# Kernel tuning notes

Hardware: AMD Instinct MI355X
Metric: run time of the kernel (lower is better)

Reference implementation:

```python
import jax, jax.numpy as jnp
import numpy as np

B, S, H, I, E = 2, 1024, 1024, 4096, 8

def setup_inputs() -> dict:
    key = jax.random.key(0)
    ks = jax.random.split(key, 8)
    s_h = 1.0 / np.sqrt(H)
    s_i = 1.0 / np.sqrt(I)
    return {
        "x": jax.random.normal(ks[0], (B, S, H), dtype=jnp.float32),
        "router_w": jax.random.uniform(ks[1], (H, E), jnp.float32, -s_h, s_h),
        "router_b": jax.random.uniform(ks[2], (E,), jnp.float32, -s_h, s_h),
        "w1": jax.random.uniform(ks[3], (E, H, I), jnp.float32, -s_h, s_h),
        "b1": jax.random.uniform(ks[4], (E, I), jnp.float32, -s_h, s_h),
        "w2": jax.random.uniform(ks[5], (E, I, H), jnp.float32, -s_i, s_i),
        "b2": jax.random.uniform(ks[6], (E, H), jnp.float32, -s_i, s_i),
        "game_emb": jax.random.normal(ks[7], (E, H), dtype=jnp.float32) * 0.02,
    }

def reference(x, router_w, router_b, w1, b1, w2, b2, game_emb):
    # Router: top-1 expert per token (softmax is monotone, argmax of logits)
    logits = jnp.einsum('bsh,he->bse', x, router_w) + router_b  # [B,S,E]
    expert_idx = jnp.argmax(logits, axis=-1)                    # [B,S] int
    out = jnp.zeros_like(x)
    n_experts = w1.shape[0]
    for e in range(n_experts):  # fixed small expert loop
        mask = (expert_idx == e)[..., None]                     # [B,S,1]
        sel = x + 0.1 * game_emb[e]                             # embedding add
        h = jax.nn.gelu(jnp.einsum('bsh,hi->bsi', sel, w1[e]) + b1[e], approximate=False)
        y = jnp.einsum('bsi,ih->bsh', h, w2[e]) + b2[e]
        out = jnp.where(mask, y, out)                           # scatter combine
    return out
```

## Files before the change

kernel.cpp:

```cpp
#include <hip/hip_runtime.h>
#include <hip/hip_bf16.h>
#include <math.h>

#define HDIM 1024
#define IDIM 4096
#define NE 8
#define NTOK 2048
#define PADROWS 256

typedef __attribute__((ext_vector_type(8))) short bf16x8;
typedef __attribute__((ext_vector_type(4))) float f32x4;

__device__ __forceinline__ unsigned int f2bf(float f) {
    unsigned int u = __float_as_uint(f);
    u = (u + 0x7FFFu + ((u >> 16) & 1u)) >> 16;
    return u;
}

__device__ __forceinline__ unsigned int pkbf2(float lo, float hi) {
    union { __hip_bfloat162 h; unsigned int u; } cv;
    cv.h = __float22bfloat162_rn(make_float2(lo, hi));
    return cv.u;
}

__device__ __forceinline__ float comp4(const float4& v, int c) {
    return c == 0 ? v.x : c == 1 ? v.y : c == 2 ? v.z : v.w;
}

__device__ __forceinline__ int swz8(int i) { return (i ^ (i >> 3)) & 7; }

__device__ __forceinline__ float gelu_erf(float v) {
    float x = v * 0.70710678118654752f;
    float ax = fabsf(x);
    float t = 1.0f / (1.0f + 0.3275911f * ax);
    float p = t * (0.254829592f + t * (-0.284496736f + t * (1.421413741f +
              t * (-1.453152027f + t * 1.061405429f))));
    float er = 1.0f - p * __expf(-x * x);
    er = copysignf(er, v);
    return 0.5f * v * (1.0f + er);
}

template<typename T, typename U>
__device__ __forceinline__ void gld16(const T* g, U* l) {
    __builtin_amdgcn_global_load_lds((const __attribute__((address_space(1))) void*)g,
                                     (__attribute__((address_space(3))) void*)l, 16, 0, 0);
}

__global__ __launch_bounds__(256) void router_k(const float* __restrict__ x,
                                                const float* __restrict__ rw,
                                                const float* __restrict__ rb,
                                                int* __restrict__ eidx,
                                                int* __restrict__ counts) {
    const int wave = threadIdx.x >> 6, lane = threadIdx.x & 63;
    const int t = blockIdx.x * 4 + wave;
    if (t >= NTOK) return;
    double acc[NE];
#pragma unroll
    for (int e = 0; e < NE; e++) acc[e] = 0.0;
    for (int h = lane; h < HDIM; h += 64) {
        double xv = (double)x[(size_t)t * HDIM + h];
        const float4* rwp = (const float4*)&rw[h * NE];
        float4 r0 = rwp[0], r1 = rwp[1];
        acc[0] += xv * (double)r0.x;  acc[1] += xv * (double)r0.y;
        acc[2] += xv * (double)r0.z;  acc[3] += xv * (double)r0.w;
        acc[4] += xv * (double)r1.x;  acc[5] += xv * (double)r1.y;
        acc[6] += xv * (double)r1.z;  acc[7] += xv * (double)r1.w;
    }
#pragma unroll
    for (int m = 32; m >= 1; m >>= 1) {
#pragma unroll
        for (int e = 0; e < NE; e++) acc[e] += __shfl_xor(acc[e], m);
    }
    if (lane == 0) {
        double best = acc[0] + (double)rb[0];
        int be = 0;
#pragma unroll
        for (int e = 1; e < NE; e++) {
            double v = acc[e] + (double)rb[e];
            if (v > best) { best = v; be = e; }
        }
        eidx[t] = be;
        atomicAdd(&counts[be], 1);
    }
}

__global__ void scan_k(const int* __restrict__ counts, int* __restrict__ offsets) {
    if (threadIdx.x == 0 && blockIdx.x == 0) {
        int s = 0;
        for (int e = 0; e < NE; e++) { offsets[e] = s; s += counts[e]; }
        offsets[NE] = s;
    }
}

__global__ __launch_bounds__(256) void gather_k(const float* __restrict__ x,
                                                const float* __restrict__ gemb,
                                                const int* __restrict__ eidx,
                                                const int* __restrict__ offsets,
                                                int* __restrict__ cursors,
                                                int* __restrict__ rowmap,
                                                unsigned short* __restrict__ Xg) {
    __shared__ int srow, se;
    const int t = blockIdx.x;
    if (threadIdx.x == 0) {
        int e = eidx[t];
        int pos = atomicAdd(&cursors[e], 1);
        int row = offsets[e] + pos;
        rowmap[row] = t;
        srow = row; se = e;
    }
    __syncthreads();
    const int row = srow, e = se;
    const int c = threadIdx.x * 4;
    float4 xv = *(const float4*)&x[(size_t)t * HDIM + c];
    float4 gv = *(const float4*)&gemb[(size_t)e * HDIM + c];
    ushort4 o;
    o.x = (unsigned short)f2bf(xv.x + 0.1f * gv.x);
    o.y = (unsigned short)f2bf(xv.y + 0.1f * gv.y);
    o.z = (unsigned short)f2bf(xv.z + 0.1f * gv.z);
    o.w = (unsigned short)f2bf(xv.w + 0.1f * gv.w);
    *(ushort4*)&Xg[(size_t)row * HDIM + c] = o;
}

template<int EPI>
__global__ __launch_bounds__(256, 3) void moe_gemm_k(
        const unsigned short* __restrict__ A, int lda, int Kfull, int ksplit,
        const float* __restrict__ Bw, int ldbN,
        const float* __restrict__ bias,
        const int* __restrict__ offsets, const int* __restrict__ rowmap,
        unsigned short* __restrict__ Hout, float* __restrict__ Yout,
        float* __restrict__ P, size_t pstride) {
    __shared__ __align__(16) unsigned short At[2][128 * 64];
    __shared__ __align__(16) unsigned short Bt[128 * 64];

    const int e = blockIdx.z & 7;
    const int split = blockIdx.z >> 3;
    const int rend = offsets[e + 1];
    const int r0 = offsets[e] + blockIdx.y * 128;
    if (r0 >= rend) return;
    const int c0 = blockIdx.x * 128;
    const int kbeg = split * ksplit;
    const int nt = ksplit / 64;
    const float* Be = Bw + (size_t)e * Kfull * ldbN;

    const int tid = threadIdx.x;
    const int wave = tid >> 6, lane = tid & 63;
    const int wr = (wave >> 1) * 64, wc = (wave & 1) * 64;
    const int l15 = lane & 15, l4 = lane >> 4;

    const int bcol = (tid & 31) * 4;
    const int boct = tid >> 5;
    const float* bsrc = Be + (size_t)boct * 8 * ldbN + c0 + bcol;
    int bwo[4];
#pragma unroll
    for (int i = 0; i < 4; ++i) {
        int col = bcol + i;
        bwo[i] = col * 64 + (boct ^ swz8(col)) * 8;
    }

    const unsigned short* adsrc[4];
    int adoff[4];
#pragma unroll
    for (int p = 0; p < 4; ++p) {
        int gidx = p * 256 + tid;
        int row = gidx >> 3, ps = gidx & 7;
        adsrc[p] = A + (size_t)(r0 + row) * lda + (ps ^ swz8(row)) * 8;
        adoff[p] = gidx * 8;
    }

    float4 fv[8];
    auto loadB = [&](int kabs) {
#pragma unroll
        for (int j = 0; j < 8; ++j)
            fv[j] = *(const float4*)&bsrc[(size_t)(kabs + j) * ldbN];
    };
    auto dmaA = [&](int kabs, int buf) {
#pragma unroll
        for (int p = 0; p < 4; ++p)
            gld16(adsrc[p] + kabs, &At[buf][adoff[p]]);
    };

    f32x4 acc[4][4];
#pragma unroll
    for (int m = 0; m < 4; ++m)
#pragma unroll
        for (int n = 0; n < 4; ++n) acc[m][n] = (f32x4){0.f, 0.f, 0.f, 0.f};

    loadB(kbeg);
    dmaA(kbeg, 0);
    for (int t = 0; t < nt; ++t) {
        const int cur = t & 1;
#pragma unroll
        for (int i = 0; i < 4; ++i) {
            uint4 w;
            w.x = pkbf2(comp4(fv[0], i), comp4(fv[1], i));
            w.y = pkbf2(comp4(fv[2], i), comp4(fv[3], i));
            w.z = pkbf2(comp4(fv[4], i), comp4(fv[5], i));
            w.w = pkbf2(comp4(fv[6], i), comp4(fv[7], i));
            *(uint4*)&Bt[bwo[i]] = w;
        }
        if (t + 1 < nt) {
            loadB(kbeg + (t + 1) * 64);
            dmaA(kbeg + (t + 1) * 64, cur ^ 1);
            asm volatile("s_waitcnt vmcnt(12) lgkmcnt(0)" ::: "memory");
        } else {
            asm volatile("s_waitcnt vmcnt(0) lgkmcnt(0)" ::: "memory");
        }
        __builtin_amdgcn_s_barrier();
        __builtin_amdgcn_sched_barrier(0);
#pragma unroll
        for (int kh = 0; kh < 2; ++kh) {
            const int kb = kh * 4 + l4;
            bf16x8 af[4], bfr[4];
#pragma unroll
            for (int m = 0; m < 4; ++m) {
                int row = wr + m * 16 + l15;
                af[m] = *(const bf16x8*)&At[cur][row * 64 + (kb ^ swz8(row)) * 8];
            }
#pragma unroll
            for (int n = 0; n < 4; ++n) {
                int col = wc + n * 16 + l15;
                bfr[n] = *(const bf16x8*)&Bt[col * 64 + (kb ^ swz8(col)) * 8];
            }
#pragma unroll
            for (int m = 0; m < 4; ++m)
#pragma unroll
                for (int n = 0; n < 4; ++n)
                    acc[m][n] = __builtin_amdgcn_mfma_f32_16x16x32_bf16(af[m], bfr[n], acc[m][n], 0, 0, 0);
        }
        __builtin_amdgcn_sched_barrier(0);
        __builtin_amdgcn_s_barrier();
        __builtin_amdgcn_sched_barrier(0);
    }

#pragma unroll
    for (int m = 0; m < 4; ++m) {
#pragma unroll
        for (int r = 0; r < 4; ++r) {
            const int row = r0 + wr + m * 16 + l4 * 4 + r;
            if (row < rend) {
                if constexpr (EPI == 0) {
#pragma unroll
                    for (int n = 0; n < 4; ++n) {
                        int col = c0 + wc + n * 16 + l15;
                        float v = acc[m][n][r] + bias[(size_t)e * ldbN + col];
                        Hout[(size_t)row * IDIM + col] = (unsigned short)f2bf(gelu_erf(v));
                    }
                } else if (split == 0) {
                    const int tt = rowmap[row];
#pragma unroll
                    for (int n = 0; n < 4; ++n) {
                        int col = c0 + wc + n * 16 + l15;
                        Yout[(size_t)tt * HDIM + col] = acc[m][n][r] + bias[(size_t)e * ldbN + col];
                    }
                } else {
                    float* Ps = P + (size_t)(split - 1) * pstride;
#pragma unroll
                    for (int n = 0; n < 4; ++n) {
                        int col = c0 + wc + n * 16 + l15;
                        Ps[(size_t)row * HDIM + col] = acc[m][n][r];
                    }
                }
            }
        }
    }
}

__global__ __launch_bounds__(256) void reduce_k(const float* __restrict__ P,
                                                size_t pstride, int nparts,
                                                const int* __restrict__ rowmap,
                                                float* __restrict__ out) {
    const int row = blockIdx.x;
    const int t = rowmap[row];
    const int c = threadIdx.x * 4;
    f32x4 s = *(const f32x4*)&out[(size_t)t * HDIM + c];
    for (int p = 0; p < nparts; ++p)
        s += *(const f32x4*)&P[(size_t)p * pstride + (size_t)row * HDIM + c];
    *(f32x4*)&out[(size_t)t * HDIM + c] = s;
}

extern "C" void kernel_launch(void* const* d_in, const int* in_sizes, int n_in,
                              void* d_out, int out_size, void* d_ws, size_t ws_size,
                              hipStream_t stream) {
    const float* x    = (const float*)d_in[0];
    const float* rw   = (const float*)d_in[1];
    const float* rb   = (const float*)d_in[2];
    const float* w1   = (const float*)d_in[3];
    const float* b1   = (const float*)d_in[4];
    const float* w2   = (const float*)d_in[5];
    const float* b2   = (const float*)d_in[6];
    const float* gemb = (const float*)d_in[7];
    float* out = (float*)d_out;

    char* ws = (char*)d_ws;
    int* meta    = (int*)ws;
    int* counts  = meta;
    int* cursors = meta + 8;
    int* offsets = meta + 16;
    int* eidx    = meta + 32;
    int* rowmap  = meta + 32 + NTOK;
    size_t off = 32768;
    unsigned short* Xg = (unsigned short*)(ws + off);
    off += (size_t)(NTOK + PADROWS) * HDIM * 2;
    unsigned short* Hbuf = (unsigned short*)(ws + off);
    off += (size_t)(NTOK + PADROWS) * IDIM * 2;
    float* P = (float*)(ws + off);
    const size_t pstride = (size_t)NTOK * HDIM;
    int nsplit = 1;
    if (ws_size >= off + 3 * pstride * 4) nsplit = 4;
    else if (ws_size >= off + 1 * pstride * 4) nsplit = 2;

    hipMemsetAsync(counts, 0, 16 * sizeof(int), stream);
    router_k<<<NTOK / 4, 256, 0, stream>>>(x, rw, rb, eidx, counts);
    scan_k<<<1, 64, 0, stream>>>(counts, offsets);
    gather_k<<<NTOK, 256, 0, stream>>>(x, gemb, eidx, offsets, cursors, rowmap, Xg);
    moe_gemm_k<0><<<dim3(IDIM / 128, 3, NE), 256, 0, stream>>>(
        Xg, HDIM, HDIM, HDIM, w1, IDIM, b1, offsets, rowmap, Hbuf, nullptr, nullptr, 0);
    moe_gemm_k<1><<<dim3(HDIM / 128, 3, NE * nsplit), 256, 0, stream>>>(
        Hbuf, IDIM, IDIM, IDIM / nsplit, w2, HDIM, b2, offsets, rowmap, nullptr, out, P, pstride);
    if (nsplit > 1)
        reduce_k<<<NTOK, 256, 0, stream>>>(P, pstride, nsplit - 1, rowmap, out);
}
```

Before: 193.6 us.

## Prefetch second-layer expert weights into cache during first GEMM

The first expert GEMM now issues extra global-to-LDS loads that sweep the whole w2 weight tensor into a dummy shared buffer. The aim is to warm the large last-level cache so the second GEMM reads w2 from cache instead of HBM. This adds memory traffic and in-flight loads to the first GEMM, which may already be bandwidth-bound. Blocks that exit early skip their share of the prefetch.

```diff
diff --git a/kernel.cpp b/kernel.cpp
--- a/kernel.cpp
+++ b/kernel.cpp
@@ -121,16 +121,18 @@
     *(ushort4*)&Xg[(size_t)row * HDIM + c] = o;
 }
 
-template<int EPI>
+template<int EPI, int TOUCH>
 __global__ __launch_bounds__(256, 3) void moe_gemm_k(
         const unsigned short* __restrict__ A, int lda, int Kfull, int ksplit,
         const float* __restrict__ Bw, int ldbN,
         const float* __restrict__ bias,
         const int* __restrict__ offsets, const int* __restrict__ rowmap,
         unsigned short* __restrict__ Hout, float* __restrict__ Yout,
-        float* __restrict__ P, size_t pstride) {
+        float* __restrict__ P, size_t pstride,
+        const float* __restrict__ tw) {
     __shared__ __align__(16) unsigned short At[2][128 * 64];
     __shared__ __align__(16) unsigned short Bt[128 * 64];
+    __shared__ __align__(16) float Dummy[TOUCH ? 1024 : 16];
 
     const int e = blockIdx.z & 7;
     const int split = blockIdx.z >> 3;
@@ -147,6 +149,21 @@
     const int wr = (wave >> 1) * 64, wc = (wave & 1) * 64;
     const int l15 = lane & 15, l4 = lane >> 4;
 
+    const float* tbase = nullptr;
+    float* tdst = nullptr;
+    if constexpr (TOUCH) {
+        int fid = blockIdx.x + 32 * (blockIdx.y + 3 * blockIdx.z);
+        tbase = tw + (size_t)fid * 43648 + tid * 4;
+        tdst = &Dummy[tid * 4];
+    }
+    auto touch = [&](int b) {
+        if constexpr (TOUCH) {
+#pragma unroll
+            for (int i = 0; i < 4; ++i)
+                gld16(tbase + (size_t)(b * 4 + i) * 1024, tdst);
+        }
+    };
+
     const int bcol = (tid & 31) * 4;
     const int boct = tid >> 5;
     const float* bsrc = Be + (size_t)boct * 8 * ldbN + c0 + bcol;
@@ -187,6 +204,7 @@
 
     loadB(kbeg);
     dmaA(kbeg, 0);
+    touch(16);
     for (int t = 0; t < nt; ++t) {
         const int cur = t & 1;
 #pragma unroll
@@ -201,7 +219,11 @@
         if (t + 1 < nt) {
             loadB(kbeg + (t + 1) * 64);
             dmaA(kbeg + (t + 1) * 64, cur ^ 1);
-            asm volatile("s_waitcnt vmcnt(12) lgkmcnt(0)" ::: "memory");
+            touch(t);
+            if constexpr (TOUCH)
+                asm volatile("s_waitcnt vmcnt(20) lgkmcnt(0)" ::: "memory");
+            else
+                asm volatile("s_waitcnt vmcnt(12) lgkmcnt(0)" ::: "memory");
         } else {
             asm volatile("s_waitcnt vmcnt(0) lgkmcnt(0)" ::: "memory");
         }
@@ -313,10 +335,12 @@
     router_k<<<NTOK / 4, 256, 0, stream>>>(x, rw, rb, eidx, counts);
     scan_k<<<1, 64, 0, stream>>>(counts, offsets);
     gather_k<<<NTOK, 256, 0, stream>>>(x, gemb, eidx, offsets, cursors, rowmap, Xg);
-    moe_gemm_k<0><<<dim3(IDIM / 128, 3, NE), 256, 0, stream>>>(
-        Xg, HDIM, HDIM, HDIM, w1, IDIM, b1, offsets, rowmap, Hbuf, nullptr, nullptr, 0);
-    moe_gemm_k<1><<<dim3(HDIM / 128, 3, NE * nsplit), 256, 0, stream>>>(
-        Hbuf, IDIM, IDIM, IDIM / nsplit, w2, HDIM, b2, offsets, rowmap, nullptr, out, P, pstride);
+    moe_gemm_k<0, 1><<<dim3(IDIM / 128, 3, NE), 256, 0, stream>>>(
+        Xg, HDIM, HDIM, HDIM, w1, IDIM, b1, offsets, rowmap,
+        Hbuf, nullptr, nullptr, 0, w2);
+    moe_gemm_k<1, 0><<<dim3(HDIM / 128, 3, NE * nsplit), 256, 0, stream>>>(
+        Hbuf, IDIM, IDIM, IDIM / nsplit, w2, HDIM, b2, offsets, rowmap,
+        nullptr, out, P, pstride, nullptr);
     if (nsplit > 1)
         reduce_k<<<NTOK, 256, 0, stream>>>(P, pstride, nsplit - 1, rowmap, out);
 }
```

New measurement: 214.9 us. 11.0% more time.
